# Kernel tuning notes

Measured on AMD Instinct MI355X. Metric: run time of the kernel, lower is better.

## Reference

```python
import jax, jax.numpy as jnp
import numpy as np

B, N, D, H = 8, 8192, 512, 8  # batch, seq, hidden, heads
DH = D // H


def _rope_tables(n, d, dtype=jnp.float32):
    # standard rotate-half RoPE tables over the full hidden dim (d/2 freq pairs)
    half = d // 2
    inv_freq = 1.0 / (10000.0 ** (np.arange(0, half, dtype=np.float32) / half))
    pos = np.arange(n, dtype=np.float32)
    ang = np.einsum('n,f->nf', pos, inv_freq)          # [N, D/2]
    ang = np.concatenate([ang, ang], axis=-1)          # [N, D]
    return jnp.asarray(np.cos(ang), dtype), jnp.asarray(np.sin(ang), dtype)


def setup_inputs() -> dict:
    key = jax.random.key(0)
    k1, k2 = jax.random.split(key)
    hidden_states = jax.random.normal(k1, (B, N, D), dtype=jnp.float32)
    num_layers = 24
    std = 0.02 / np.sqrt(2.0 * num_layers * D)
    W = jax.random.normal(k2, (D, D), dtype=jnp.float32) * std
    cos, sin = _rope_tables(N, D)
    return {"hidden_states": hidden_states, "W": W, "cos": cos, "sin": sin}


def _rotate_half(x):
    x1, x2 = jnp.split(x, 2, axis=-1)
    return jnp.concatenate([-x2, x1], axis=-1)


def reference(hidden_states, W, cos, sin):
    # dropout(p=0) in eval mode -> identity
    x = hidden_states * cos + _rotate_half(hidden_states) * sin  # RoPE, [B,N,D]
    q = jnp.einsum('bnd,ed->bne', x, W)                          # F.linear(x, W)
    qh = q.reshape(B, N, H, DH)
    xh = x.reshape(B, N, H, DH)
    # linear-complexity path: (K^T V) then Q @ (.), per head
    kv = jnp.einsum('bnhd,bnhe->bhde', xh, xh)   # [B,H,DH,DH]
    out = jnp.einsum('bnhd,bhde->bnhe', qh, kv)  # [B,N,H,DH]
    return out.reshape(B, N, D)
```

## Files before the change

kernel.cpp:

```cpp
#include <hip/hip_runtime.h>
#include <hip/hip_bf16.h>
#include <stdint.h>

#define BB 8
#define NN 8192
#define DD 512
#define HH 8
#define DHD 64
#define NCH 32

typedef __attribute__((ext_vector_type(8))) short bf16x8;
typedef __attribute__((ext_vector_type(4))) float f32x4;
typedef __attribute__((ext_vector_type(16))) float f32x16;
typedef __attribute__((ext_vector_type(4))) float f4v;

__device__ __forceinline__ unsigned short f2bf(float f) {
  union { float f; unsigned int u; } v; v.f = f;
  return (unsigned short)((v.u + 0x7FFFu + ((v.u >> 16) & 1u)) >> 16);
}

__device__ __forceinline__ unsigned cvtpk(float lo, float hi) {
  unsigned r;
  asm("v_cvt_pk_bf16_f32 %0, %1, %2" : "=v"(r) : "v"(lo), "v"(hi));
  return r;
}

__device__ __forceinline__ void async16(const void* g, void* l) {
  __builtin_amdgcn_global_load_lds(
      (const __attribute__((address_space(1))) void*)g,
      (__attribute__((address_space(3))) void*)l, 16, 0, 0);
}

__global__ __launch_bounds__(1024, 4) void ropekv_kernel(
    const float* __restrict__ h, const float* __restrict__ cs,
    const float* __restrict__ sn, unsigned short* __restrict__ x,
    float* __restrict__ kvp, int nbh) {
  __shared__ __align__(16) unsigned int xt32[2][512 * 34];
  int blk = blockIdx.x;
  int chunk = blk & 31, b = blk >> 5;
  int tid = threadIdx.x;
  int wave = tid >> 6, lane = tid & 63;
  int rpar = lane & 1;
  int g = lane >> 1;
  int cf = g * 8;
  int l15 = lane & 15, q = lane >> 4;
  int head = wave >> 1;
  int half = wave & 1;
  int hd = head * 64;
  size_t row0 = (size_t)b * NN + (size_t)chunk * 256;
  int n0 = chunk * 256;

  f32x4 acc[2][4];
#pragma unroll
  for (int i = 0; i < 2; ++i)
#pragma unroll
    for (int j = 0; j < 4; ++j) acc[i][j] = (f32x4){0.f, 0.f, 0.f, 0.f};

  f4v ha[2][2], hb[2][2];

  auto loadt = [&](int t) {
#pragma unroll
    for (int p = 0; p < 2; ++p) {
      int r = 2 * (wave + 16 * p) + rpar;
      const float* hp = h + (row0 + t * 64 + r) * DD + cf;
      ha[p][0] = __builtin_nontemporal_load((const f4v*)hp);
      ha[p][1] = __builtin_nontemporal_load((const f4v*)(hp + 4));
      hb[p][0] = __builtin_nontemporal_load((const f4v*)(hp + 256));
      hb[p][1] = __builtin_nontemporal_load((const f4v*)(hp + 260));
    }
  };

  auto ropet = [&](int t) {
    int pb = t & 1;
#pragma unroll
    for (int p = 0; p < 2; ++p) {
      int r = 2 * (wave + 16 * p) + rpar;
      int nr = n0 + t * 64 + r;
      const float* cp = cs + (size_t)nr * DD + cf;
      const float* sp = sn + (size_t)nr * DD + cf;
      f4v c0 = *(const f4v*)cp, c1 = *(const f4v*)(cp + 4);
      f4v s0 = *(const f4v*)sp, s1 = *(const f4v*)(sp + 4);
      f4v xl0 = ha[p][0] * c0 - hb[p][0] * s0;
      f4v xl1 = ha[p][1] * c1 - hb[p][1] * s1;
      f4v xh0 = hb[p][0] * c0 + ha[p][0] * s0;
      f4v xh1 = hb[p][1] * c1 + ha[p][1] * s1;
      unsigned ml[4], mh[4];
      ml[0] = cvtpk(xl0.x, xl0.y);
      ml[1] = cvtpk(xl0.z, xl0.w);
      ml[2] = cvtpk(xl1.x, xl1.y);
      ml[3] = cvtpk(xl1.z, xl1.w);
      mh[0] = cvtpk(xh0.x, xh0.y);
      mh[1] = cvtpk(xh0.z, xh0.w);
      mh[2] = cvtpk(xh1.x, xh1.y);
      mh[3] = cvtpk(xh1.z, xh1.w);
      unsigned short* xp = x + (row0 + t * 64 + r) * DD + cf;
      uint4 st0; st0.x = ml[0]; st0.y = ml[1]; st0.z = ml[2]; st0.w = ml[3];
      uint4 st1; st1.x = mh[0]; st1.y = mh[1]; st1.z = mh[2]; st1.w = mh[3];
      *(uint4*)xp         = st0;
      *(uint4*)(xp + 256) = st1;
      unsigned pk[8];
#pragma unroll
      for (int k = 0; k < 4; ++k) {
        unsigned mine = rpar ? mh[k] : ml[k];
        unsigned send = rpar ? ml[k] : mh[k];
        unsigned recv = (unsigned)__shfl_xor((int)send, 1, 64);
        if (!rpar) {
          pk[2 * k]     = (mine & 0xffffu) | (recv << 16);
          pk[2 * k + 1] = (mine >> 16) | (recv & 0xffff0000u);
        } else {
          pk[2 * k]     = (recv & 0xffffu) | (mine << 16);
          pk[2 * k + 1] = (recv >> 16) | (mine & 0xffff0000u);
        }
      }
      int np = wave + 16 * p;
      int dbase = cf + (rpar ? 256 : 0);
      int rot = (g >> 1) & 7;
#pragma unroll
      for (int w = 0; w < 8; ++w) {
        int jj = (w + rot) & 7;
        xt32[pb][(dbase + jj) * 34 + np] = pk[jj];
      }
    }
  };

  auto mfmat = [&](int t) {
    const unsigned short* xt16 = (const unsigned short*)xt32[t & 1];
#pragma unroll
    for (int ks = 0; ks < 64; ks += 32) {
      bf16x8 af[2], bf[4];
#pragma unroll
      for (int i = 0; i < 2; ++i)
        af[i] = *(const bf16x8*)&xt16[(hd + half * 32 + i * 16 + l15) * 68 + ks + q * 8];
#pragma unroll
      for (int j = 0; j < 4; ++j)
        bf[j] = *(const bf16x8*)&xt16[(hd + j * 16 + l15) * 68 + ks + q * 8];
#pragma unroll
      for (int i = 0; i < 2; ++i)
#pragma unroll
        for (int j = 0; j < 4; ++j)
          acc[i][j] = __builtin_amdgcn_mfma_f32_16x16x32_bf16(af[i], bf[j], acc[i][j], 0, 0, 0);
    }
  };

  loadt(0);
  ropet(0);
  loadt(1);
  __syncthreads();
#pragma unroll
  for (int t = 0; t < 4; ++t) {
    if (t < 3) ropet(t + 1);
    if (t < 2) loadt(t + 2);
    mfmat(t);
    __syncthreads();
  }

  int bh = b * 8 + head;
  float* dst = kvp + ((size_t)chunk * nbh + bh) * 4096;
#pragma unroll
  for (int i = 0; i < 2; ++i)
#pragma unroll
    for (int j = 0; j < 4; ++j)
#pragma unroll
      for (int reg = 0; reg < 4; ++reg)
        dst[(half * 32 + i * 16 + q * 4 + reg) * 64 + j * 16 + l15] = acc[i][j][reg];
}

__global__ __launch_bounds__(512, 2) void wkvt_kernel(
    const float* __restrict__ W, const float* __restrict__ kvp,
    unsigned short* __restrict__ wkvt, int nbh) {
  __shared__ float kvs[64 * 16];
  __shared__ __align__(16) float ws[64 * 512];
  int blk = blockIdx.x;
  int bh = blk >> 2, eq = blk & 3;
  int b = bh >> 3, hh = bh & 7;
  int tid = threadIdx.x;
  if (tid < 256) {
    int idx = tid * 4;
    int d = idx >> 4, ec = idx & 15;
    f4v s = (f4v){0.f, 0.f, 0.f, 0.f};
    for (int c = 0; c < NCH; ++c)
      s += *(const f4v*)&kvp[((size_t)c * nbh + bh) * 4096 + d * 64 + eq * 16 + ec];
    *(f4v*)&kvs[idx] = s;
  }
#pragma unroll
  for (int i = 0; i < 16; ++i) {
    int idx = i * 2048 + tid * 4;
    *(f4v*)&ws[idx] = *(const f4v*)&W[(size_t)(hh * DHD + (idx >> 9)) * DD + (idx & 511)];
  }
  __syncthreads();
  int el = tid & 15, fg = tid >> 4;
  f4v av[4];
#pragma unroll
  for (int k = 0; k < 4; ++k) av[k] = (f4v){0.f, 0.f, 0.f, 0.f};
#pragma unroll 8
  for (int d = 0; d < 64; ++d) {
    float kvv = kvs[d * 16 + el];
    const f4v* wr = (const f4v*)&ws[d * DD + fg * 16];
#pragma unroll
    for (int k = 0; k < 4; ++k) av[k] += wr[k] * kvv;
  }
  unsigned short tb[16];
#pragma unroll
  for (int k = 0; k < 4; ++k) {
    tb[k * 4 + 0] = f2bf(av[k].x); tb[k * 4 + 1] = f2bf(av[k].y);
    tb[k * 4 + 2] = f2bf(av[k].z); tb[k * 4 + 3] = f2bf(av[k].w);
  }
  size_t ob = ((size_t)b * DD + hh * DHD + eq * 16 + el) * DD + fg * 16;
  *(uint4*)&wkvt[ob]     = *(uint4*)&tb[0];
  *(uint4*)&wkvt[ob + 8] = *(uint4*)&tb[8];
}

__global__ __launch_bounds__(256, 4) void gemm_kernel(const unsigned short* __restrict__ x,
                                                      const unsigned short* __restrict__ wkvt,
                                                      float* __restrict__ out) {
  __shared__ __align__(16) unsigned short As[128 * 64];
  __shared__ __align__(16) unsigned short Bs[128 * 64];
  int mt = blockIdx.x, ct = blockIdx.y, bz = blockIdx.z;
  int tid = threadIdx.x, wave = tid >> 6, lane = tid & 63;
  int wm = wave & 1, wn = wave >> 1;
  int l31 = lane & 31, hk = lane >> 5;
  const unsigned short* Ag = x    + ((size_t)bz * NN + mt * 128) * DD;
  const unsigned short* Bg = wkvt + ((size_t)bz * DD + ct * 128) * DD;

  int su_row[4], su_ss[4];
#pragma unroll
  for (int i = 0; i < 4; ++i) {
    int u = i * 256 + tid;
    su_row[i] = u >> 3;
    su_ss[i]  = (u & 7) ^ ((u >> 3) & 7);
  }

  f32x16 acc[2][2];
#pragma unroll
  for (int mi = 0; mi < 2; ++mi)
#pragma unroll
    for (int ni = 0; ni < 2; ++ni)
#pragma unroll
      for (int r = 0; r < 16; ++r) acc[mi][ni][r] = 0.f;

  for (int kk = 0; kk < 512; kk += 64) {
#pragma unroll
    for (int i = 0; i < 4; ++i) {
      int u = i * 256 + tid;
      async16(Ag + (size_t)su_row[i] * DD + kk + su_ss[i] * 8, &As[u * 8]);
      async16(Bg + (size_t)su_row[i] * DD + kk + su_ss[i] * 8, &Bs[u * 8]);
    }
    __syncthreads();
#pragma unroll
    for (int ks = 0; ks < 64; ks += 16) {
      bf16x8 a[2], bb[2];
#pragma unroll
      for (int mi = 0; mi < 2; ++mi) {
        int row = wm * 64 + mi * 32 + l31;
        int s = ((ks >> 3) + hk) ^ (row & 7);
        a[mi] = *(const bf16x8*)&As[row * 64 + s * 8];
      }
#pragma unroll
      for (int ni = 0; ni < 2; ++ni) {
        int row = wn * 64 + ni * 32 + l31;
        int s = ((ks >> 3) + hk) ^ (row & 7);
        bb[ni] = *(const bf16x8*)&Bs[row * 64 + s * 8];
      }
#pragma unroll
      for (int mi = 0; mi < 2; ++mi)
#pragma unroll
        for (int ni = 0; ni < 2; ++ni)
          acc[mi][ni] = __builtin_amdgcn_mfma_f32_32x32x16_bf16(a[mi], bb[ni], acc[mi][ni], 0, 0, 0);
    }
    __syncthreads();
  }
  float* ob = out + ((size_t)bz * NN + mt * 128) * DD + ct * 128;
#pragma unroll
  for (int mi = 0; mi < 2; ++mi)
#pragma unroll
    for (int ni = 0; ni < 2; ++ni)
#pragma unroll
      for (int r = 0; r < 16; ++r) {
        int row = wm * 64 + mi * 32 + (r & 3) + 8 * (r >> 2) + 4 * hk;
        int col = wn * 64 + ni * 32 + l31;
        __builtin_nontemporal_store(acc[mi][ni][r], &ob[(size_t)row * DD + col]);
      }
}

extern "C" void kernel_launch(void* const* d_in, const int* in_sizes, int n_in,
                              void* d_out, int out_size, void* d_ws, size_t ws_size,
                              hipStream_t stream) {
  (void)in_sizes; (void)n_in; (void)out_size;
  const float* h  = (const float*)d_in[0];
  const float* W  = (const float*)d_in[1];
  const float* cs = (const float*)d_in[2];
  const float* sn = (const float*)d_in[3];
  float* out = (float*)d_out;

  const size_t x_full     = (size_t)BB * NN * DD * 2;
  const size_t kvp_full   = (size_t)NCH * BB * HH * DHD * DHD * 4;
  const size_t wkvt_full  = (size_t)BB * DD * DD * 2;
  const size_t x_batch    = (size_t)NN * DD * 2;
  const size_t kvp_batch  = (size_t)NCH * HH * DHD * DHD * 4;
  const size_t wkvt_batch = (size_t)DD * DD * 2;

  if (ws_size >= x_full + kvp_full + wkvt_full) {
    unsigned short* xw   = (unsigned short*)d_ws;
    float*          kvp  = (float*)((char*)d_ws + x_full);
    unsigned short* wkvt = (unsigned short*)((char*)d_ws + x_full + kvp_full);
    ropekv_kernel<<<dim3(BB * 32), dim3(1024), 0, stream>>>(h, cs, sn, xw, kvp, BB * HH);
    wkvt_kernel<<<dim3(BB * HH * 4), dim3(512), 0, stream>>>(W, kvp, wkvt, BB * HH);
    gemm_kernel<<<dim3(NN / 128, DD / 128, BB), dim3(256), 0, stream>>>(xw, wkvt, out);
  } else {
    unsigned short* xw   = (unsigned short*)d_ws;
    float*          kvp  = (float*)((char*)d_ws + x_batch);
    unsigned short* wkvt = (unsigned short*)((char*)d_ws + x_batch + kvp_batch);
    for (int b = 0; b < BB; ++b) {
      ropekv_kernel<<<dim3(32), dim3(1024), 0, stream>>>(
          h + (size_t)b * NN * DD, cs, sn, xw, kvp, HH);
      wkvt_kernel<<<dim3(HH * 4), dim3(512), 0, stream>>>(W, kvp, wkvt, HH);
      gemm_kernel<<<dim3(NN / 128, DD / 128, 1), dim3(256), 0, stream>>>(
          xw, wkvt, out + (size_t)b * NN * DD);
    }
  }
}
```

Measured before the change: 310.7 us.

## Halve ropekv block to 512 threads with one head per wave, single LDS buffer

The RoPE+KV kernel now uses 8 waves per block instead of 16, so each wave computes the full 64x64 KV tile for one head and reuses the same A fragments as B operands. Each wave handles twice as many rows per tile in two load/rope groups, and the double-buffered LDS transpose becomes a single buffer with an extra barrier per tile. This cuts LDS fragment reads and LDS footprint, which may allow more blocks per CU. In exchange it gives up the overlap between rope of the next tile and MFMA of the current one, and leaves fewer threads to hide global load latency.

```diff
diff --git a/kernel.cpp b/kernel.cpp
--- a/kernel.cpp
+++ b/kernel.cpp
@@ -31,11 +31,11 @@
       (__attribute__((address_space(3))) void*)l, 16, 0, 0);
 }
 
-__global__ __launch_bounds__(1024, 4) void ropekv_kernel(
+__global__ __launch_bounds__(512, 4) void ropekv_kernel(
     const float* __restrict__ h, const float* __restrict__ cs,
     const float* __restrict__ sn, unsigned short* __restrict__ x,
     float* __restrict__ kvp, int nbh) {
-  __shared__ __align__(16) unsigned int xt32[2][512 * 34];
+  __shared__ __align__(16) unsigned int xt32[512 * 34];
   int blk = blockIdx.x;
   int chunk = blk & 31, b = blk >> 5;
   int tid = threadIdx.x;
@@ -44,24 +44,23 @@
   int g = lane >> 1;
   int cf = g * 8;
   int l15 = lane & 15, q = lane >> 4;
-  int head = wave >> 1;
-  int half = wave & 1;
-  int hd = head * 64;
+  int hd = wave * 64;
   size_t row0 = (size_t)b * NN + (size_t)chunk * 256;
   int n0 = chunk * 256;
 
-  f32x4 acc[2][4];
-#pragma unroll
-  for (int i = 0; i < 2; ++i)
+  f32x4 acc[4][4];
+#pragma unroll
+  for (int i = 0; i < 4; ++i)
 #pragma unroll
     for (int j = 0; j < 4; ++j) acc[i][j] = (f32x4){0.f, 0.f, 0.f, 0.f};
 
   f4v ha[2][2], hb[2][2];
 
-  auto loadt = [&](int t) {
+  auto loadG = [&](int t, int gr) {
 #pragma unroll
     for (int p = 0; p < 2; ++p) {
-      int r = 2 * (wave + 16 * p) + rpar;
+      int pp = gr * 2 + p;
+      int r = 2 * (wave + 8 * pp) + rpar;
       const float* hp = h + (row0 + t * 64 + r) * DD + cf;
       ha[p][0] = __builtin_nontemporal_load((const f4v*)hp);
       ha[p][1] = __builtin_nontemporal_load((const f4v*)(hp + 4));
@@ -70,11 +69,11 @@
     }
   };
 
-  auto ropet = [&](int t) {
-    int pb = t & 1;
+  auto ropeG = [&](int t, int gr) {
 #pragma unroll
     for (int p = 0; p < 2; ++p) {
-      int r = 2 * (wave + 16 * p) + rpar;
+      int pp = gr * 2 + p;
+      int r = 2 * (wave + 8 * pp) + rpar;
       int nr = n0 + t * 64 + r;
       const float* cp = cs + (size_t)nr * DD + cf;
       const float* sp = sn + (size_t)nr * DD + cf;
@@ -112,57 +111,53 @@
           pk[2 * k + 1] = (recv >> 16) | (mine & 0xffff0000u);
         }
       }
-      int np = wave + 16 * p;
+      int np = wave + 8 * pp;
       int dbase = cf + (rpar ? 256 : 0);
       int rot = (g >> 1) & 7;
 #pragma unroll
       for (int w = 0; w < 8; ++w) {
         int jj = (w + rot) & 7;
-        xt32[pb][(dbase + jj) * 34 + np] = pk[jj];
+        xt32[(dbase + jj) * 34 + np] = pk[jj];
       }
     }
   };
 
-  auto mfmat = [&](int t) {
-    const unsigned short* xt16 = (const unsigned short*)xt32[t & 1];
+  auto mfmat = [&]() {
+    const unsigned short* xt16 = (const unsigned short*)xt32;
 #pragma unroll
     for (int ks = 0; ks < 64; ks += 32) {
-      bf16x8 af[2], bf[4];
-#pragma unroll
-      for (int i = 0; i < 2; ++i)
-        af[i] = *(const bf16x8*)&xt16[(hd + half * 32 + i * 16 + l15) * 68 + ks + q * 8];
-#pragma unroll
-      for (int j = 0; j < 4; ++j)
-        bf[j] = *(const bf16x8*)&xt16[(hd + j * 16 + l15) * 68 + ks + q * 8];
-#pragma unroll
-      for (int i = 0; i < 2; ++i)
+      bf16x8 af[4];
+#pragma unroll
+      for (int i = 0; i < 4; ++i)
+        af[i] = *(const bf16x8*)&xt16[(hd + i * 16 + l15) * 68 + ks + q * 8];
+#pragma unroll
+      for (int i = 0; i < 4; ++i)
 #pragma unroll
         for (int j = 0; j < 4; ++j)
-          acc[i][j] = __builtin_amdgcn_mfma_f32_16x16x32_bf16(af[i], bf[j], acc[i][j], 0, 0, 0);
+          acc[i][j] = __builtin_amdgcn_mfma_f32_16x16x32_bf16(af[i], af[j], acc[i][j], 0, 0, 0);
     }
   };
 
-  loadt(0);
-  ropet(0);
-  loadt(1);
-  __syncthreads();
-#pragma unroll
+  loadG(0, 0);
   for (int t = 0; t < 4; ++t) {
-    if (t < 3) ropet(t + 1);
-    if (t < 2) loadt(t + 2);
-    mfmat(t);
+    ropeG(t, 0);
+    loadG(t, 1);
+    ropeG(t, 1);
+    if (t < 3) loadG(t + 1, 0);
     __syncthreads();
-  }
-
-  int bh = b * 8 + head;
+    mfmat();
+    __syncthreads();
+  }
+
+  int bh = b * 8 + wave;
   float* dst = kvp + ((size_t)chunk * nbh + bh) * 4096;
 #pragma unroll
-  for (int i = 0; i < 2; ++i)
+  for (int i = 0; i < 4; ++i)
 #pragma unroll
     for (int j = 0; j < 4; ++j)
 #pragma unroll
       for (int reg = 0; reg < 4; ++reg)
-        dst[(half * 32 + i * 16 + q * 4 + reg) * 64 + j * 16 + l15] = acc[i][j][reg];
+        dst[(i * 16 + q * 4 + reg) * 64 + j * 16 + l15] = acc[i][j][reg];
 }
 
 __global__ __launch_bounds__(512, 2) void wkvt_kernel(
@@ -303,7 +298,7 @@
     unsigned short* xw   = (unsigned short*)d_ws;
     float*          kvp  = (float*)((char*)d_ws + x_full);
     unsigned short* wkvt = (unsigned short*)((char*)d_ws + x_full + kvp_full);
-    ropekv_kernel<<<dim3(BB * 32), dim3(1024), 0, stream>>>(h, cs, sn, xw, kvp, BB * HH);
+    ropekv_kernel<<<dim3(BB * 32), dim3(512), 0, stream>>>(h, cs, sn, xw, kvp, BB * HH);
     wkvt_kernel<<<dim3(BB * HH * 4), dim3(512), 0, stream>>>(W, kvp, wkvt, BB * HH);
     gemm_kernel<<<dim3(NN / 128, DD / 128, BB), dim3(256), 0, stream>>>(xw, wkvt, out);
   } else {
@@ -311,7 +306,7 @@
     float*          kvp  = (float*)((char*)d_ws + x_batch);
     unsigned short* wkvt = (unsigned short*)((char*)d_ws + x_batch + kvp_batch);
     for (int b = 0; b < BB; ++b) {
-      ropekv_kernel<<<dim3(32), dim3(1024), 0, stream>>>(
+      ropekv_kernel<<<dim3(32), dim3(512), 0, stream>>>(
           h + (size_t)b * NN * DD, cs, sn, xw, kvp, HH);
       wkvt_kernel<<<dim3(HH * 4), dim3(512), 0, stream>>>(W, kvp, wkvt, HH);
       gemm_kernel<<<dim3(NN / 128, DD / 128, 1), dim3(256), 0, stream>>>(
```

After: 365.0 us. +17.5%, slower.
